# Kernel optimization log

Hardware: AMD Instinct MI355X
Metric: run time of the kernel (lower is better)

The kernel has to match this reference:

```python
import jax, jax.numpy as jnp
import numpy as np


def dct_matrices(N):
    # torch_dct-style unnormalized DCT-II (norm=None): X_k = 2 * sum_n x_n cos(pi*(2n+1)k/(2N))
    n = jnp.arange(N, dtype=jnp.float32)
    ang = jnp.pi * (2.0 * n[None, :] + 1.0) * n[:, None] / (2.0 * N)  # [k, n]
    D = 2.0 * jnp.cos(ang)                                            # forward DCT matrix [k, n]
    w = jnp.where(n == 0, 0.5, 1.0)                                   # half-weight on DC term
    M = (jnp.cos(ang).T * w[None, :]) / (2.0 * N)                     # inverse DCT matrix [n, k]
    return D, M


def setup_inputs() -> dict:
    key = jax.random.key(0)
    k1, k2, k3 = jax.random.split(key, 3)
    B, c_in, c_out, H, W, kh, kw = 8, 64, 128, 128, 128, 5, 5
    K = float(np.sqrt(1.0 / (c_in * kh * kw)))
    x = jax.random.normal(k1, (B, c_in, H, W), dtype=jnp.float32)
    weight = (2.0 * jax.random.uniform(k2, (c_out, c_in, kh, kw), dtype=jnp.float32) - 1.0) * K
    bias = (2.0 * jax.random.uniform(k3, (c_out,), dtype=jnp.float32) - 1.0) * K
    return {"x": x, "weight": weight, "bias": bias}


def reference(x, weight, bias):
    B, c_in, H, W = x.shape
    c_out, _, kh, kw = weight.shape
    D, M = dct_matrices(H)

    # DCT-II along H axis of input
    xd = jnp.einsum('kh,bchw->bckw', D, x)            # (B, c_in, H, W)
    xf = jnp.fft.rfft(xd, axis=-1)                    # (B, c_in, H, Wf) complex

    # Pad kernel along H to full size, DCT along H, rFFT along W with n=W
    wpad = jnp.pad(weight, ((0, 0), (0, 0), (0, H - kh), (0, 0)))
    wd = jnp.einsum('kh,oihw->oikw', D, wpad)         # (c_out, c_in, H, kw)
    wf = jnp.fft.rfft(wd, n=W, axis=-1)               # (c_out, c_in, H, Wf) complex

    # Broadcast complex multiply + reduce over c_in (fused via einsum)
    hf = jnp.einsum('bchw,ochw->bohw', xf, wf)        # (B, c_out, H, Wf)
    h = jnp.fft.irfft(hf, n=W, axis=-1)               # (B, c_out, H, W)

    # Inverse DCT along H, add bias, stride slice (stride = 1)
    h = jnp.einsum('nk,bokw->bonw', M, h) + bias[None, :, None, None]
    return h[:, :, ::1, ::1]
```

## Files before the change

### kernel.cpp

```cpp
#include <hip/hip_runtime.h>


using half8v = __attribute__((ext_vector_type(8))) _Float16;
using half4v = __attribute__((ext_vector_type(4))) _Float16;
using f32x4  = __attribute__((ext_vector_type(4))) float;

#define PI_F 3.14159265358979323846f

__device__ __forceinline__ int sw_off(int n, int k, int K, int mask) {
    int c = k >> 3;
    return n * K + (((c ^ (n & mask)) << 3) | (k & 7));
}

__global__ __launch_bounds__(256) void k_wd(const float* __restrict__ w,
                                            _Float16* __restrict__ WD,
                                            _Float16* __restrict__ D,
                                            _Float16* __restrict__ M) {
    __shared__ float lw[1600];
    __shared__ float lcos[320];
    int bid = blockIdx.x;
    int co = bid >> 1, k0 = (bid & 1) << 6;
    int tid = threadIdx.x;

    if (bid < 128 && tid < 128) {
        int k = bid, h = tid;
        float ang = PI_F * (float)((2 * h + 1) * k) * (1.0f / 256.0f);
        float c = cosf(ang);
        D[k * 128 + h] = (_Float16)(2.0f * c);
        float wk = (k == 0) ? 0.5f : 1.0f;
        M[h * 128 + k] = (_Float16)(c * wk * (1.0f / 256.0f));
    }

    for (int e = tid; e < 1600; e += 256) lw[e] = w[co * 1600 + e];
    for (int e = tid; e < 320; e += 256) {
        int kl = e / 5, i = e - kl * 5;
        lcos[e] = 2.0f * cosf(PI_F * (float)((2 * i + 1) * (k0 + kl)) * (1.0f / 256.0f));
    }
    __syncthreads();

    for (int e = tid; e < 20480; e += 256) {
        int kk = e & 31, rest = e >> 5;
        int s = rest % 10, kl = rest / 10;
        int j = s >> 1, ci = ((s & 1) << 5) + kk;
        const float* wp = &lw[ci * 25 + j];
        const float* cp = &lcos[kl * 5];
        float acc = 0.f;
#pragma unroll
        for (int i = 0; i < 5; ++i) acc += cp[i] * wp[i * 5];
        WD[(((long)(k0 + kl) * 10 + s) * 128 + co) * 32 + kk] = (_Float16)acc;
    }
}

__device__ __forceinline__ void gemm128_gA_T(const _Float16* __restrict__ gA,
                                             const _Float16* lB,
                                             f32x4 acc[4][4], int tid) {
    int lane = tid & 63, ln = lane & 15, q = lane >> 4;
    int wave = tid >> 6, wm = wave >> 1, wn = wave & 1;
#pragma unroll
    for (int s = 0; s < 4; ++s) {
        half8v af[4], bf[4];
#pragma unroll
        for (int mt = 0; mt < 4; ++mt) {
            int m = wm * 64 + mt * 16 + ln;
            af[mt] = *(const half8v*)(&gA[m * 128 + (s * 4 + q) * 8]);
        }
#pragma unroll
        for (int nt = 0; nt < 4; ++nt) {
            int n = wn * 64 + nt * 16 + ln;
            bf[nt] = *(const half8v*)(&lB[n * 128 + (((s * 4 + q) ^ (n & 15)) << 3)]);
        }
#pragma unroll
        for (int mt = 0; mt < 4; ++mt)
#pragma unroll
            for (int nt = 0; nt < 4; ++nt)
                acc[mt][nt] = __builtin_amdgcn_mfma_f32_16x16x32_f16(bf[nt], af[mt], acc[mt][nt], 0, 0, 0);
    }
}

__device__ __forceinline__ void stage_transB64(const _Float16* __restrict__ src, int row_stride,
                                               _Float16* l, int tid) {
    int kb = tid >> 4, wb = tid & 15;
    int k0 = kb * 4, w0 = wb * 8;
    half8v r0 = *(const half8v*)(&src[(k0 + 0) * row_stride + w0]);
    half8v r1 = *(const half8v*)(&src[(k0 + 1) * row_stride + w0]);
    half8v r2 = *(const half8v*)(&src[(k0 + 2) * row_stride + w0]);
    half8v r3 = *(const half8v*)(&src[(k0 + 3) * row_stride + w0]);
#pragma unroll
    for (int dw = 0; dw < 8; ++dw) {
        int n = w0 + dw;
        half4v p = {r0[dw], r1[dw], r2[dw], r3[dw]};
        *(half4v*)(&l[sw_off(n, k0, 64, 7)]) = p;
    }
}

__device__ __forceinline__ void stage_transB128(const _Float16* __restrict__ src, int row_stride,
                                                _Float16* l, int tid) {
    int blkA = tid, blkB = tid + 256;
    int kA = (blkA >> 4) * 4, wA = (blkA & 15) * 8;
    int kB = (blkB >> 4) * 4, wB = (blkB & 15) * 8;
    half8v a0 = *(const half8v*)(&src[(kA + 0) * row_stride + wA]);
    half8v a1 = *(const half8v*)(&src[(kA + 1) * row_stride + wA]);
    half8v a2 = *(const half8v*)(&src[(kA + 2) * row_stride + wA]);
    half8v a3 = *(const half8v*)(&src[(kA + 3) * row_stride + wA]);
    half8v b0 = *(const half8v*)(&src[(kB + 0) * row_stride + wB]);
    half8v b1 = *(const half8v*)(&src[(kB + 1) * row_stride + wB]);
    half8v b2 = *(const half8v*)(&src[(kB + 2) * row_stride + wB]);
    half8v b3 = *(const half8v*)(&src[(kB + 3) * row_stride + wB]);
#pragma unroll
    for (int dw = 0; dw < 8; ++dw) {
        half4v p = {a0[dw], a1[dw], a2[dw], a3[dw]};
        *(half4v*)(&l[sw_off(wA + dw, kA, 128, 15)]) = p;
    }
#pragma unroll
    for (int dw = 0; dw < 8; ++dw) {
        half4v p = {b0[dw], b1[dw], b2[dw], b3[dw]};
        *(half4v*)(&l[sw_off(wB + dw, kB, 128, 15)]) = p;
    }
}

__global__ __launch_bounds__(256) void k_dctH(const float* __restrict__ x,
                                              const _Float16* __restrict__ Dg,
                                              _Float16* __restrict__ xd) {
    __shared__ _Float16 lB[128 * 128];
    int b = blockIdx.x >> 6, ci = blockIdx.x & 63;
    int tid = threadIdx.x;

    const float* xs = x + (long)(b * 64 + ci) * 16384;
#pragma unroll
    for (int rep = 0; rep < 2; ++rep) {
        int blk = tid + rep * 256;
        int hb = blk >> 4, wb = blk & 15;
        int h0 = hb * 4, w0 = wb * 8;
        f32x4 f[4][2];
#pragma unroll
        for (int dh = 0; dh < 4; ++dh) {
            f[dh][0] = *(const f32x4*)(&xs[(h0 + dh) * 128 + w0]);
            f[dh][1] = *(const f32x4*)(&xs[(h0 + dh) * 128 + w0 + 4]);
        }
#pragma unroll
        for (int dw = 0; dw < 8; ++dw) {
            int n = w0 + dw;
            half4v p = {(_Float16)f[0][dw >> 2][dw & 3], (_Float16)f[1][dw >> 2][dw & 3],
                        (_Float16)f[2][dw >> 2][dw & 3], (_Float16)f[3][dw >> 2][dw & 3]};
            *(half4v*)(&lB[sw_off(n, h0, 128, 15)]) = p;
        }
    }
    __syncthreads();

    f32x4 acc[4][4] = {};
    gemm128_gA_T(Dg, lB, acc, tid);

    int lane = tid & 63, ln = lane & 15, q = lane >> 4;
    int wave = tid >> 6, wm = wave >> 1, wn = wave & 1;
#pragma unroll
    for (int mt = 0; mt < 4; ++mt)
#pragma unroll
        for (int nt = 0; nt < 4; ++nt) {
            int kk = wm * 64 + mt * 16 + ln;
            int w0 = wn * 64 + nt * 16 + q * 4;
            half4v p = {(_Float16)acc[mt][nt][0], (_Float16)acc[mt][nt][1],
                        (_Float16)acc[mt][nt][2], (_Float16)acc[mt][nt][3]};
            *(half4v*)(&xd[((long)(kk * 8 + b) * 64 + ci) * 128 + w0]) = p;
        }
}

__global__ __launch_bounds__(256) void k_conv(const _Float16* __restrict__ xd,
                                              const _Float16* __restrict__ WD,
                                              _Float16* __restrict__ y2) {
    __shared__ _Float16 lX[128 * 64];
    int bid = blockIdx.x;
    int k = bid & 127, b = bid >> 7;
    int tid = threadIdx.x;

    const _Float16* xs = xd + (long)(k * 8 + b) * 8192;
    stage_transB64(xs, 128, lX, tid);
    __syncthreads();

    int lane = tid & 63, ln = lane & 15, q = lane >> 4;
    int wave = tid >> 6, wm = wave >> 1, wn = wave & 1;
    f32x4 acc[4][4] = {};

    const _Float16* wkb = WD + (long)k * 40960;

    for (int s = 0; s < 10; ++s) {
        int j = s >> 1;
        int cb = (s & 1) << 2;
        const _Float16* wt = wkb + s * 4096;
        half8v af[4], bf[4];
#pragma unroll
        for (int mt = 0; mt < 4; ++mt) {
            int m = wm * 64 + mt * 16 + ln;
            af[mt] = *(const half8v*)(&wt[m * 32 + q * 8]);
        }
#pragma unroll
        for (int nt = 0; nt < 4; ++nt) {
            int wcol = wn * 64 + nt * 16 + ln;
            int n = (wcol - j) & 127;
            bf[nt] = *(const half8v*)(&lX[n * 64 + (((cb + q) ^ (n & 7)) << 3)]);
        }
#pragma unroll
        for (int mt = 0; mt < 4; ++mt)
#pragma unroll
            for (int nt = 0; nt < 4; ++nt)
                acc[mt][nt] = __builtin_amdgcn_mfma_f32_16x16x32_f16(bf[nt], af[mt], acc[mt][nt], 0, 0, 0);
    }

    _Float16* yb = y2 + (long)(b * 128 + k) * 16384;
#pragma unroll
    for (int mt = 0; mt < 4; ++mt)
#pragma unroll
        for (int nt = 0; nt < 4; ++nt) {
            int co = wm * 64 + mt * 16 + ln;
            int w0 = wn * 64 + nt * 16 + q * 4;
            half4v p = {(_Float16)acc[mt][nt][0], (_Float16)acc[mt][nt][1],
                        (_Float16)acc[mt][nt][2], (_Float16)acc[mt][nt][3]};
            *(half4v*)(&yb[co * 128 + w0]) = p;
        }
}

__global__ __launch_bounds__(256) void k_idct(const _Float16* __restrict__ y2,
                                              const _Float16* __restrict__ Mg,
                                              const float* __restrict__ bias,
                                              float* __restrict__ out) {
    __shared__ _Float16 lB[128 * 128];
    int b = blockIdx.x >> 7, co = blockIdx.x & 127;
    int tid = threadIdx.x;

    const _Float16* src = y2 + (long)b * 2097152 + co * 128;
    stage_transB128(src, 16384, lB, tid);
    __syncthreads();

    f32x4 acc[4][4] = {};
    gemm128_gA_T(Mg, lB, acc, tid);

    float bv = bias[co];
    float* ob = out + ((long)(b * 128 + co)) * 16384;
    int lane = tid & 63, ln = lane & 15, q = lane >> 4;
    int wave = tid >> 6, wm = wave >> 1, wn = wave & 1;
#pragma unroll
    for (int mt = 0; mt < 4; ++mt)
#pragma unroll
        for (int nt = 0; nt < 4; ++nt) {
            int h = wm * 64 + mt * 16 + ln;
            int w0 = wn * 64 + nt * 16 + q * 4;
            f32x4 p = {acc[mt][nt][0] + bv, acc[mt][nt][1] + bv,
                       acc[mt][nt][2] + bv, acc[mt][nt][3] + bv};
            *(f32x4*)(&ob[h * 128 + w0]) = p;
        }
}

extern "C" void kernel_launch(void* const* d_in, const int* in_sizes, int n_in,
                              void* d_out, int out_size, void* d_ws, size_t ws_size,
                              hipStream_t stream) {
    const float* x    = (const float*)d_in[0];
    const float* w    = (const float*)d_in[1];
    const float* bias = (const float*)d_in[2];
    float* out = (float*)d_out;

    char* ws = (char*)d_ws;
    _Float16* D  = (_Float16*)(ws);
    _Float16* M  = (_Float16*)(ws + 32768);
    _Float16* WD = (_Float16*)(ws + 65536);
    _Float16* xd = (_Float16*)(ws + 65536 + 10485760);
    _Float16* y2 = (_Float16*)(ws + 65536 + 10485760 + 16777216);

    k_wd  <<<dim3(256),  dim3(256), 0, stream>>>(w, WD, D, M);
    k_dctH<<<dim3(512),  dim3(256), 0, stream>>>(x, D, xd);
    k_conv<<<dim3(1024), dim3(256), 0, stream>>>(xd, WD, y2);
    k_idct<<<dim3(1024), dim3(256), 0, stream>>>(y2, M, bias, out);
}
```

Baseline: 150.2 us.

## Merge weight-DCT and input-DCT kernels, compute DCT basis inline, split W halves

Folds the weight-transform kernel and the input DCT-along-H kernel into one launch, with extra blocks handling the weight work. Both phases share one shared-memory union. The input DCT no longer reads a precomputed D matrix; it evaluates the cosine coefficients in registers. Both the DCT and IDCT kernels now split W into two 64-column halves, doubling block count and halving shared memory per block. This removes one launch and the serialization between weight prep and input DCT. The cost is many cosf calls per MFMA fragment in the DCT phase and less reuse of operand A per block.

```diff
diff --git a/kernel.cpp b/kernel.cpp
--- a/kernel.cpp
+++ b/kernel.cpp
@@ -12,125 +12,53 @@
     return n * K + (((c ^ (n & mask)) << 3) | (k & 7));
 }
 
-__global__ __launch_bounds__(256) void k_wd(const float* __restrict__ w,
-                                            _Float16* __restrict__ WD,
-                                            _Float16* __restrict__ D,
-                                            _Float16* __restrict__ M) {
-    __shared__ float lw[1600];
-    __shared__ float lcos[320];
+__global__ __launch_bounds__(256) void k_prep(const float* __restrict__ x,
+                                              const float* __restrict__ w,
+                                              _Float16* __restrict__ xd,
+                                              _Float16* __restrict__ WD,
+                                              _Float16* __restrict__ M) {
+    __shared__ union {
+        _Float16 lB[64 * 128];
+        struct { float lw[1600]; float lcos[320]; } wd;
+    } sm;
     int bid = blockIdx.x;
-    int co = bid >> 1, k0 = (bid & 1) << 6;
     int tid = threadIdx.x;
 
-    if (bid < 128 && tid < 128) {
-        int k = bid, h = tid;
-        float ang = PI_F * (float)((2 * h + 1) * k) * (1.0f / 256.0f);
-        float c = cosf(ang);
-        D[k * 128 + h] = (_Float16)(2.0f * c);
-        float wk = (k == 0) ? 0.5f : 1.0f;
-        M[h * 128 + k] = (_Float16)(c * wk * (1.0f / 256.0f));
-    }
-
-    for (int e = tid; e < 1600; e += 256) lw[e] = w[co * 1600 + e];
-    for (int e = tid; e < 320; e += 256) {
-        int kl = e / 5, i = e - kl * 5;
-        lcos[e] = 2.0f * cosf(PI_F * (float)((2 * i + 1) * (k0 + kl)) * (1.0f / 256.0f));
-    }
-    __syncthreads();
-
-    for (int e = tid; e < 20480; e += 256) {
-        int kk = e & 31, rest = e >> 5;
-        int s = rest % 10, kl = rest / 10;
-        int j = s >> 1, ci = ((s & 1) << 5) + kk;
-        const float* wp = &lw[ci * 25 + j];
-        const float* cp = &lcos[kl * 5];
-        float acc = 0.f;
-#pragma unroll
-        for (int i = 0; i < 5; ++i) acc += cp[i] * wp[i * 5];
-        WD[(((long)(k0 + kl) * 10 + s) * 128 + co) * 32 + kk] = (_Float16)acc;
-    }
-}
-
-__device__ __forceinline__ void gemm128_gA_T(const _Float16* __restrict__ gA,
-                                             const _Float16* lB,
-                                             f32x4 acc[4][4], int tid) {
-    int lane = tid & 63, ln = lane & 15, q = lane >> 4;
-    int wave = tid >> 6, wm = wave >> 1, wn = wave & 1;
-#pragma unroll
-    for (int s = 0; s < 4; ++s) {
-        half8v af[4], bf[4];
-#pragma unroll
-        for (int mt = 0; mt < 4; ++mt) {
-            int m = wm * 64 + mt * 16 + ln;
-            af[mt] = *(const half8v*)(&gA[m * 128 + (s * 4 + q) * 8]);
-        }
-#pragma unroll
-        for (int nt = 0; nt < 4; ++nt) {
-            int n = wn * 64 + nt * 16 + ln;
-            bf[nt] = *(const half8v*)(&lB[n * 128 + (((s * 4 + q) ^ (n & 15)) << 3)]);
-        }
-#pragma unroll
-        for (int mt = 0; mt < 4; ++mt)
-#pragma unroll
-            for (int nt = 0; nt < 4; ++nt)
-                acc[mt][nt] = __builtin_amdgcn_mfma_f32_16x16x32_f16(bf[nt], af[mt], acc[mt][nt], 0, 0, 0);
-    }
-}
-
-__device__ __forceinline__ void stage_transB64(const _Float16* __restrict__ src, int row_stride,
-                                               _Float16* l, int tid) {
-    int kb = tid >> 4, wb = tid & 15;
-    int k0 = kb * 4, w0 = wb * 8;
-    half8v r0 = *(const half8v*)(&src[(k0 + 0) * row_stride + w0]);
-    half8v r1 = *(const half8v*)(&src[(k0 + 1) * row_stride + w0]);
-    half8v r2 = *(const half8v*)(&src[(k0 + 2) * row_stride + w0]);
-    half8v r3 = *(const half8v*)(&src[(k0 + 3) * row_stride + w0]);
-#pragma unroll
-    for (int dw = 0; dw < 8; ++dw) {
-        int n = w0 + dw;
-        half4v p = {r0[dw], r1[dw], r2[dw], r3[dw]};
-        *(half4v*)(&l[sw_off(n, k0, 64, 7)]) = p;
-    }
-}
-
-__device__ __forceinline__ void stage_transB128(const _Float16* __restrict__ src, int row_stride,
-                                                _Float16* l, int tid) {
-    int blkA = tid, blkB = tid + 256;
-    int kA = (blkA >> 4) * 4, wA = (blkA & 15) * 8;
-    int kB = (blkB >> 4) * 4, wB = (blkB & 15) * 8;
-    half8v a0 = *(const half8v*)(&src[(kA + 0) * row_stride + wA]);
-    half8v a1 = *(const half8v*)(&src[(kA + 1) * row_stride + wA]);
-    half8v a2 = *(const half8v*)(&src[(kA + 2) * row_stride + wA]);
-    half8v a3 = *(const half8v*)(&src[(kA + 3) * row_stride + wA]);
-    half8v b0 = *(const half8v*)(&src[(kB + 0) * row_stride + wB]);
-    half8v b1 = *(const half8v*)(&src[(kB + 1) * row_stride + wB]);
-    half8v b2 = *(const half8v*)(&src[(kB + 2) * row_stride + wB]);
-    half8v b3 = *(const half8v*)(&src[(kB + 3) * row_stride + wB]);
-#pragma unroll
-    for (int dw = 0; dw < 8; ++dw) {
-        half4v p = {a0[dw], a1[dw], a2[dw], a3[dw]};
-        *(half4v*)(&l[sw_off(wA + dw, kA, 128, 15)]) = p;
-    }
-#pragma unroll
-    for (int dw = 0; dw < 8; ++dw) {
-        half4v p = {b0[dw], b1[dw], b2[dw], b3[dw]};
-        *(half4v*)(&l[sw_off(wB + dw, kB, 128, 15)]) = p;
-    }
-}
-
-__global__ __launch_bounds__(256) void k_dctH(const float* __restrict__ x,
-                                              const _Float16* __restrict__ Dg,
-                                              _Float16* __restrict__ xd) {
-    __shared__ _Float16 lB[128 * 128];
-    int b = blockIdx.x >> 6, ci = blockIdx.x & 63;
-    int tid = threadIdx.x;
-
-    const float* xs = x + (long)(b * 64 + ci) * 16384;
-#pragma unroll
-    for (int rep = 0; rep < 2; ++rep) {
-        int blk = tid + rep * 256;
-        int hb = blk >> 4, wb = blk & 15;
-        int h0 = hb * 4, w0 = wb * 8;
+    if (bid >= 1024) {
+        int bp = bid - 1024;
+        int co = bp >> 1, k0 = (bp & 1) << 6;
+        if (bp < 128 && tid < 128) {
+            int k = bp, h = tid;
+            float ang = PI_F * (float)((2 * h + 1) * k) * (1.0f / 256.0f);
+            float wk = (k == 0) ? 0.5f : 1.0f;
+            M[h * 128 + k] = (_Float16)(cosf(ang) * wk * (1.0f / 256.0f));
+        }
+        for (int e = tid; e < 1600; e += 256) sm.wd.lw[e] = w[co * 1600 + e];
+        for (int e = tid; e < 320; e += 256) {
+            int kl = e / 5, i = e - kl * 5;
+            sm.wd.lcos[e] = 2.0f * cosf(PI_F * (float)((2 * i + 1) * (k0 + kl)) * (1.0f / 256.0f));
+        }
+        __syncthreads();
+        for (int e = tid; e < 20480; e += 256) {
+            int kk = e & 31, rest = e >> 5;
+            int s = rest % 10, kl = rest / 10;
+            int j = s >> 1, ci = ((s & 1) << 5) + kk;
+            const float* wp = &sm.wd.lw[ci * 25 + j];
+            const float* cp = &sm.wd.lcos[kl * 5];
+            float acc = 0.f;
+#pragma unroll
+            for (int i = 0; i < 5; ++i) acc += cp[i] * wp[i * 5];
+            WD[(((long)(k0 + kl) * 10 + s) * 128 + co) * 32 + kk] = (_Float16)acc;
+        }
+        return;
+    }
+
+    int b = bid >> 7, ci = (bid >> 1) & 63, wh = bid & 1;
+    const float* xs = x + (long)(b * 64 + ci) * 16384 + wh * 64;
+
+    {
+        int kb = tid >> 3, wb = tid & 7;
+        int h0 = kb * 4, w0 = wb * 8;
         f32x4 f[4][2];
 #pragma unroll
         for (int dh = 0; dh < 4; ++dh) {
@@ -142,22 +70,45 @@
             int n = w0 + dw;
             half4v p = {(_Float16)f[0][dw >> 2][dw & 3], (_Float16)f[1][dw >> 2][dw & 3],
                         (_Float16)f[2][dw >> 2][dw & 3], (_Float16)f[3][dw >> 2][dw & 3]};
-            *(half4v*)(&lB[sw_off(n, h0, 128, 15)]) = p;
+            *(half4v*)(&sm.lB[sw_off(n, h0, 128, 15)]) = p;
         }
     }
     __syncthreads();
-
-    f32x4 acc[4][4] = {};
-    gemm128_gA_T(Dg, lB, acc, tid);
 
     int lane = tid & 63, ln = lane & 15, q = lane >> 4;
     int wave = tid >> 6, wm = wave >> 1, wn = wave & 1;
+    f32x4 acc[4][2] = {};
+
+#pragma unroll
+    for (int s = 0; s < 4; ++s) {
+        half8v af[4], bf[2];
+#pragma unroll
+        for (int mt = 0; mt < 4; ++mt) {
+            int m = wm * 64 + mt * 16 + ln;
+            int h0 = s * 32 + q * 8;
+            float mf = (float)m * (PI_F / 256.0f);
+#pragma unroll
+            for (int j = 0; j < 8; ++j)
+                af[mt][j] = (_Float16)(2.0f * cosf((float)(2 * (h0 + j) + 1) * mf));
+        }
+#pragma unroll
+        for (int nt = 0; nt < 2; ++nt) {
+            int n = wn * 32 + nt * 16 + ln;
+            bf[nt] = *(const half8v*)(&sm.lB[n * 128 + (((s * 4 + q) ^ (n & 15)) << 3)]);
+        }
+#pragma unroll
+        for (int mt = 0; mt < 4; ++mt)
+#pragma unroll
+            for (int nt = 0; nt < 2; ++nt)
+                acc[mt][nt] = __builtin_amdgcn_mfma_f32_16x16x32_f16(bf[nt], af[mt], acc[mt][nt], 0, 0, 0);
+    }
+
 #pragma unroll
     for (int mt = 0; mt < 4; ++mt)
 #pragma unroll
-        for (int nt = 0; nt < 4; ++nt) {
+        for (int nt = 0; nt < 2; ++nt) {
             int kk = wm * 64 + mt * 16 + ln;
-            int w0 = wn * 64 + nt * 16 + q * 4;
+            int w0 = wh * 64 + wn * 32 + nt * 16 + q * 4;
             half4v p = {(_Float16)acc[mt][nt][0], (_Float16)acc[mt][nt][1],
                         (_Float16)acc[mt][nt][2], (_Float16)acc[mt][nt][3]};
             *(half4v*)(&xd[((long)(kk * 8 + b) * 64 + ci) * 128 + w0]) = p;
@@ -172,8 +123,21 @@
     int k = bid & 127, b = bid >> 7;
     int tid = threadIdx.x;
 
-    const _Float16* xs = xd + (long)(k * 8 + b) * 8192;
-    stage_transB64(xs, 128, lX, tid);
+    {
+        const _Float16* src = xd + (long)(k * 8 + b) * 8192;
+        int kb = tid >> 4, wb = tid & 15;
+        int k0 = kb * 4, w0 = wb * 8;
+        half8v r0 = *(const half8v*)(&src[(k0 + 0) * 128 + w0]);
+        half8v r1 = *(const half8v*)(&src[(k0 + 1) * 128 + w0]);
+        half8v r2 = *(const half8v*)(&src[(k0 + 2) * 128 + w0]);
+        half8v r3 = *(const half8v*)(&src[(k0 + 3) * 128 + w0]);
+#pragma unroll
+        for (int dw = 0; dw < 8; ++dw) {
+            int n = w0 + dw;
+            half4v p = {r0[dw], r1[dw], r2[dw], r3[dw]};
+            *(half4v*)(&lX[sw_off(n, k0, 64, 7)]) = p;
+        }
+    }
     __syncthreads();
 
     int lane = tid & 63, ln = lane & 15, q = lane >> 4;
@@ -222,27 +186,60 @@
                                               const _Float16* __restrict__ Mg,
                                               const float* __restrict__ bias,
                                               float* __restrict__ out) {
-    __shared__ _Float16 lB[128 * 128];
-    int b = blockIdx.x >> 7, co = blockIdx.x & 127;
+    __shared__ _Float16 lB[64 * 128];
+    int bid = blockIdx.x;
+    int b = bid >> 8, co = (bid >> 1) & 127, wh = bid & 1;
     int tid = threadIdx.x;
 
-    const _Float16* src = y2 + (long)b * 2097152 + co * 128;
-    stage_transB128(src, 16384, lB, tid);
+    {
+        const _Float16* src = y2 + (long)b * 2097152 + co * 128 + wh * 64;
+        int kb = tid >> 3, wb = tid & 7;
+        int k0 = kb * 4, w0 = wb * 8;
+        half8v r0 = *(const half8v*)(&src[(long)(k0 + 0) * 16384 + w0]);
+        half8v r1 = *(const half8v*)(&src[(long)(k0 + 1) * 16384 + w0]);
+        half8v r2 = *(const half8v*)(&src[(long)(k0 + 2) * 16384 + w0]);
+        half8v r3 = *(const half8v*)(&src[(long)(k0 + 3) * 16384 + w0]);
+#pragma unroll
+        for (int dw = 0; dw < 8; ++dw) {
+            int n = w0 + dw;
+            half4v p = {r0[dw], r1[dw], r2[dw], r3[dw]};
+            *(half4v*)(&lB[sw_off(n, k0, 128, 15)]) = p;
+        }
+    }
     __syncthreads();
 
-    f32x4 acc[4][4] = {};
-    gemm128_gA_T(Mg, lB, acc, tid);
+    int lane = tid & 63, ln = lane & 15, q = lane >> 4;
+    int wave = tid >> 6, wm = wave >> 1, wn = wave & 1;
+    f32x4 acc[4][2] = {};
+
+#pragma unroll
+    for (int s = 0; s < 4; ++s) {
+        half8v af[4], bf[2];
+#pragma unroll
+        for (int mt = 0; mt < 4; ++mt) {
+            int m = wm * 64 + mt * 16 + ln;
+            af[mt] = *(const half8v*)(&Mg[m * 128 + (s * 4 + q) * 8]);
+        }
+#pragma unroll
+        for (int nt = 0; nt < 2; ++nt) {
+            int n = wn * 32 + nt * 16 + ln;
+            bf[nt] = *(const half8v*)(&lB[n * 128 + (((s * 4 + q) ^ (n & 15)) << 3)]);
+        }
+#pragma unroll
+        for (int mt = 0; mt < 4; ++mt)
+#pragma unroll
+            for (int nt = 0; nt < 2; ++nt)
+                acc[mt][nt] = __builtin_amdgcn_mfma_f32_16x16x32_f16(bf[nt], af[mt], acc[mt][nt], 0, 0, 0);
+    }
 
     float bv = bias[co];
     float* ob = out + ((long)(b * 128 + co)) * 16384;
-    int lane = tid & 63, ln = lane & 15, q = lane >> 4;
-    int wave = tid >> 6, wm = wave >> 1, wn = wave & 1;
 #pragma unroll
     for (int mt = 0; mt < 4; ++mt)
 #pragma unroll
-        for (int nt = 0; nt < 4; ++nt) {
+        for (int nt = 0; nt < 2; ++nt) {
             int h = wm * 64 + mt * 16 + ln;
-            int w0 = wn * 64 + nt * 16 + q * 4;
+            int w0 = wh * 64 + wn * 32 + nt * 16 + q * 4;
             f32x4 p = {acc[mt][nt][0] + bv, acc[mt][nt][1] + bv,
                        acc[mt][nt][2] + bv, acc[mt][nt][3] + bv};
             *(f32x4*)(&ob[h * 128 + w0]) = p;
@@ -258,14 +255,12 @@
     float* out = (float*)d_out;
 
     char* ws = (char*)d_ws;
-    _Float16* D  = (_Float16*)(ws);
-    _Float16* M  = (_Float16*)(ws + 32768);
-    _Float16* WD = (_Float16*)(ws + 65536);
-    _Float16* xd = (_Float16*)(ws + 65536 + 10485760);
-    _Float16* y2 = (_Float16*)(ws + 65536 + 10485760 + 16777216);
-
-    k_wd  <<<dim3(256),  dim3(256), 0, stream>>>(w, WD, D, M);
-    k_dctH<<<dim3(512),  dim3(256), 0, stream>>>(x, D, xd);
+    _Float16* M  = (_Float16*)(ws);
+    _Float16* WD = (_Float16*)(ws + 32768);
+    _Float16* xd = (_Float16*)(ws + 32768 + 10485760);
+    _Float16* y2 = (_Float16*)(ws + 32768 + 10485760 + 16777216);
+
+    k_prep<<<dim3(1280), dim3(256), 0, stream>>>(x, w, xd, WD, M);
     k_conv<<<dim3(1024), dim3(256), 0, stream>>>(xd, WD, y2);
-    k_idct<<<dim3(1024), dim3(256), 0, stream>>>(y2, M, bias, out);
-}
+    k_idct<<<dim3(2048), dim3(256), 0, stream>>>(y2, M, bias, out);
+}
```

Measured after the change: 161.4 us. 1.07x slower.
